# Optimization experiments

Measured on AMD Instinct MI355X. Metric: run time of the kernel, lower is better.

The kernel has to match this reference:

```python
import jax, jax.numpy as jnp
import numpy as np

N = 4096          # number of leaves
M = 2 * N - 1     # total tree nodes
B = 256           # batch of distribution pairs


def setup_inputs() -> dict:
    key = jax.random.key(0)
    k0, k1, k2, k3, k4, k5 = jax.random.split(key, 6)
    # ancestor-indicator matrix: mostly zeros (structured sparse used densely)
    subtree = (jax.random.uniform(k0, (M, N)) < 0.01).astype(jnp.float32)
    d1 = jax.random.uniform(k1, (N, B), dtype=jnp.float32)
    d2 = jax.random.uniform(k2, (N, B), dtype=jnp.float32)
    ot_distances = jax.random.uniform(k3, (B,), dtype=jnp.float32)
    param = jax.random.normal(k4, (M,), dtype=jnp.float32)
    parents = jax.random.randint(k5, (M,), 0, M, dtype=jnp.int32)
    return {"d1": d1, "d2": d2, "ot_distances": ot_distances,
            "subtree": subtree, "param": param, "parents": parents}


def reference(d1, d2, ot_distances, subtree, param, parents):
    # aggregate leaf mass to every tree node: [M, B]
    m_d1 = jnp.matmul(subtree, d1)
    m_d2 = jnp.matmul(subtree, d2)
    # edge weight = parent height - node height: [M]
    w_v = param[parents] - param
    # tree-Wasserstein-1 per pair: [B]
    w1_tree = 0.5 * jnp.matmul(w_v, jnp.abs(m_d1 - m_d2))
    return jnp.sum(jnp.square(ot_distances - w1_tree))
```

## Files before the change

### kernel.cpp

```cpp
#include <hip/hip_runtime.h>

#define NN    4096
#define MM    8191
#define BB    256
#define CAP   256

__device__ __forceinline__ int prefix_lt(unsigned long long m) {
    return __builtin_amdgcn_mbcnt_hi((unsigned)(m >> 32),
           __builtin_amdgcn_mbcnt_lo((unsigned)m, 0u));
}

__device__ __forceinline__ unsigned pack2bf(float lo, float hi) {
    unsigned a = __float_as_uint(lo);
    unsigned b = __float_as_uint(hi);
    a += 0x7fffu + ((a >> 16) & 1u);
    b += 0x7fffu + ((b >> 16) & 1u);
    return (a >> 16) | (b & 0xffff0000u);
}

__global__ __launch_bounds__(256) void k_prep(const float4* __restrict__ d1,
                                              const float4* __restrict__ d2,
                                              float* __restrict__ part2,
                                              uint2* __restrict__ ddp) {
    int idx = blockIdx.x * 256 + threadIdx.x;
    if (idx < 256 * BB) part2[idx] = 0.0f;
    float4 a = d1[idx], b = d2[idx];
    uint2 r;
    r.x = pack2bf(a.x - b.x, a.y - b.y);
    r.y = pack2bf(a.z - b.z, a.w - b.w);
    ddp[idx] = r;
}

__global__ __launch_bounds__(256, 4) void k_fused(
        const float4* __restrict__ st4,
        const uint2* __restrict__ ddp,
        const float* __restrict__ param,
        const int*   __restrict__ parents,
        float* __restrict__ part2) {
    __shared__ unsigned short s_idx[4][CAP];
    __shared__ float s_part[BB];
    const int tid  = threadIdx.x;
    const int wave = tid >> 6;
    const int lane = tid & 63;
    unsigned short* buf = s_idx[wave];

    s_part[tid] = 0.0f;
    __syncthreads();

    const int m = blockIdx.x * 4 + wave;
    if (m < MM) {
        int c = 0;
        #pragma unroll
        for (int h = 0; h < 2; ++h) {
            const float4* base = st4 + (size_t)m * (NN / 4) + h * (NN / 8);
            float4 v0 = base[lane];
            float4 v1 = base[64  + lane];
            float4 v2 = base[128 + lane];
            float4 v3 = base[192 + lane];
            float4 v4 = base[256 + lane];
            float4 v5 = base[320 + lane];
            float4 v6 = base[384 + lane];
            float4 v7 = base[448 + lane];

            const int cb = h * (NN / 2);
            #define SITE(val, col)                                          \
            {                                                               \
                unsigned long long mk = __ballot((val) != 0.0f);            \
                if ((val) != 0.0f)                                          \
                    buf[c + prefix_lt(mk)] = (unsigned short)(col);         \
                c += __popcll(mk);                                          \
            }
            #define QUAD(v, cb0)                                            \
                SITE(v.x, (cb0))     SITE(v.y, (cb0) + 1)                   \
                SITE(v.z, (cb0) + 2) SITE(v.w, (cb0) + 3)
            QUAD(v0, cb + (lane)       * 4)
            QUAD(v1, cb + (64  + lane) * 4)
            QUAD(v2, cb + (128 + lane) * 4)
            QUAD(v3, cb + (192 + lane) * 4)
            QUAD(v4, cb + (256 + lane) * 4)
            QUAD(v5, cb + (320 + lane) * 4)
            QUAD(v6, cb + (384 + lane) * 4)
            QUAD(v7, cb + (448 + lane) * 4)
            #undef QUAD
            #undef SITE
        }
        __builtin_amdgcn_wave_barrier();

        float c0 = 0.f, c1 = 0.f, c2 = 0.f, c3 = 0.f;
        float e0 = 0.f, e1 = 0.f, e2 = 0.f, e3 = 0.f;
        #define UNP0(u) __uint_as_float((u) << 16)
        #define UNP1(u) __uint_as_float((u) & 0xffff0000u)
        #define ACCA(g) { c0 += UNP0(g.x); c1 += UNP1(g.x); c2 += UNP0(g.y); c3 += UNP1(g.y); }
        #define ACCB(g) { e0 += UNP0(g.x); e1 += UNP1(g.x); e2 += UNP0(g.y); e3 += UNP1(g.y); }
        const unsigned* lw = (const unsigned*)buf;
        int i = 0;
        for (; i + 8 <= c; i += 8) {
            unsigned q0 = lw[(i >> 1)    ];
            unsigned q1 = lw[(i >> 1) + 1];
            unsigned q2 = lw[(i >> 1) + 2];
            unsigned q3 = lw[(i >> 1) + 3];
            unsigned o0 = (q0 & 0xffffu) * 64u + lane;
            unsigned o1 = (q0 >> 16)     * 64u + lane;
            unsigned o2 = (q1 & 0xffffu) * 64u + lane;
            unsigned o3 = (q1 >> 16)     * 64u + lane;
            unsigned o4 = (q2 & 0xffffu) * 64u + lane;
            unsigned o5 = (q2 >> 16)     * 64u + lane;
            unsigned o6 = (q3 & 0xffffu) * 64u + lane;
            unsigned o7 = (q3 >> 16)     * 64u + lane;
            uint2 g0 = ddp[o0];
            uint2 g1 = ddp[o1];
            uint2 g2 = ddp[o2];
            uint2 g3 = ddp[o3];
            uint2 g4 = ddp[o4];
            uint2 g5 = ddp[o5];
            uint2 g6 = ddp[o6];
            uint2 g7 = ddp[o7];
            ACCA(g0) ACCB(g1) ACCA(g2) ACCB(g3)
            ACCA(g4) ACCB(g5) ACCA(g6) ACCB(g7)
        }
        for (; i + 4 <= c; i += 4) {
            unsigned q0 = lw[(i >> 1)    ];
            unsigned q1 = lw[(i >> 1) + 1];
            unsigned o0 = (q0 & 0xffffu) * 64u + lane;
            unsigned o1 = (q0 >> 16)     * 64u + lane;
            unsigned o2 = (q1 & 0xffffu) * 64u + lane;
            unsigned o3 = (q1 >> 16)     * 64u + lane;
            uint2 g0 = ddp[o0];
            uint2 g1 = ddp[o1];
            uint2 g2 = ddp[o2];
            uint2 g3 = ddp[o3];
            ACCA(g0) ACCB(g1) ACCA(g2) ACCB(g3)
        }
        for (; i < c; ++i) {
            unsigned n = buf[i];
            uint2 g = ddp[n * 64u + lane];
            ACCA(g)
        }
        #undef ACCA
        #undef ACCB
        #undef UNP0
        #undef UNP1

        const float wgt = param[parents[m]] - param[m];
        atomicAdd(&s_part[4 * lane + 0], wgt * fabsf(c0 + e0));
        atomicAdd(&s_part[4 * lane + 1], wgt * fabsf(c1 + e1));
        atomicAdd(&s_part[4 * lane + 2], wgt * fabsf(c2 + e2));
        atomicAdd(&s_part[4 * lane + 3], wgt * fabsf(c3 + e3));
    }
    __syncthreads();
    atomicAdd(&part2[(size_t)(blockIdx.x & 255) * BB + tid], s_part[tid]);
}

__global__ __launch_bounds__(1024) void k_finalize(const float* __restrict__ part2,
                                                   const float* __restrict__ ot,
                                                   float* __restrict__ out) {
    __shared__ float s_red[4][BB];
    __shared__ float s_sq[16];
    const int tid = threadIdx.x;
    const int s = tid >> 8, b = tid & 255;

    float a0 = 0.f, a1 = 0.f, a2 = 0.f, a3 = 0.f;
    float a4 = 0.f, a5 = 0.f, a6 = 0.f, a7 = 0.f;
    #pragma unroll
    for (int j = 0; j < 64; j += 8) {
        int row = s * 64 + j;
        a0 += part2[(row    ) * BB + b];
        a1 += part2[(row + 1) * BB + b];
        a2 += part2[(row + 2) * BB + b];
        a3 += part2[(row + 3) * BB + b];
        a4 += part2[(row + 4) * BB + b];
        a5 += part2[(row + 5) * BB + b];
        a6 += part2[(row + 6) * BB + b];
        a7 += part2[(row + 7) * BB + b];
    }
    s_red[s][b] = ((a0 + a1) + (a2 + a3)) + ((a4 + a5) + (a6 + a7));
    __syncthreads();

    float v = 0.0f;
    if (s == 0) {
        float w1 = (s_red[0][b] + s_red[1][b]) + (s_red[2][b] + s_red[3][b]);
        float e = ot[b] - 0.5f * w1;
        v = e * e;
    }
    #pragma unroll
    for (int off = 32; off > 0; off >>= 1) v += __shfl_down(v, off, 64);
    if ((tid & 63) == 0) s_sq[tid >> 6] = v;
    __syncthreads();
    if (tid == 0) out[0] = (s_sq[0] + s_sq[1]) + (s_sq[2] + s_sq[3]);
}

extern "C" void kernel_launch(void* const* d_in, const int* in_sizes, int n_in,
                              void* d_out, int out_size, void* d_ws, size_t ws_size,
                              hipStream_t stream) {
    const float* d1      = (const float*)d_in[0];
    const float* d2      = (const float*)d_in[1];
    const float* ot      = (const float*)d_in[2];
    const float* subtree = (const float*)d_in[3];
    const float* param   = (const float*)d_in[4];
    const int*   parents = (const int*)d_in[5];

    char* wsb = (char*)d_ws;
    float* part2 = (float*)wsb;
    uint2* ddp   = (uint2*)(wsb + 256 * BB * 4);

    k_prep<<<1024, 256, 0, stream>>>((const float4*)d1, (const float4*)d2,
                                     part2, ddp);
    k_fused<<<2048, 256, 0, stream>>>((const float4*)subtree, ddp,
                                      param, parents, part2);
    k_finalize<<<1, 1024, 0, stream>>>(part2, ot, (float*)d_out);
}
```

Measured before the change: 48.68 us.

## Make fused kernel persistent with double-buffered nontemporal subtree row loads

Shrinks the grid so each wave processes four rows, prefetching the next half-row of the subtree matrix into a second register set while compacting and gathering the current half. Subtree loads use nontemporal hints to avoid evicting the packed difference data used by the gathers. Per-row LDS atomics are replaced by register accumulation with a single atomic flush per wave. Fewer resident waves may reduce latency hiding, and register pressure rises from holding two row buffers.

```diff
diff --git a/kernel.cpp b/kernel.cpp
--- a/kernel.cpp
+++ b/kernel.cpp
@@ -4,6 +4,8 @@
 #define MM    8191
 #define BB    256
 #define CAP   256
+
+typedef float nfloat4 __attribute__((ext_vector_type(4)));
 
 __device__ __forceinline__ int prefix_lt(unsigned long long m) {
     return __builtin_amdgcn_mbcnt_hi((unsigned)(m >> 32),
@@ -32,7 +34,7 @@
 }
 
 __global__ __launch_bounds__(256, 4) void k_fused(
-        const float4* __restrict__ st4,
+        const nfloat4* __restrict__ st4,
         const uint2* __restrict__ ddp,
         const float* __restrict__ param,
         const int*   __restrict__ parents,
@@ -47,106 +49,137 @@
     s_part[tid] = 0.0f;
     __syncthreads();
 
-    const int m = blockIdx.x * 4 + wave;
-    if (m < MM) {
-        int c = 0;
-        #pragma unroll
-        for (int h = 0; h < 2; ++h) {
-            const float4* base = st4 + (size_t)m * (NN / 4) + h * (NN / 8);
-            float4 v0 = base[lane];
-            float4 v1 = base[64  + lane];
-            float4 v2 = base[128 + lane];
-            float4 v3 = base[192 + lane];
-            float4 v4 = base[256 + lane];
-            float4 v5 = base[320 + lane];
-            float4 v6 = base[384 + lane];
-            float4 v7 = base[448 + lane];
-
-            const int cb = h * (NN / 2);
-            #define SITE(val, col)                                          \
-            {                                                               \
-                unsigned long long mk = __ballot((val) != 0.0f);            \
-                if ((val) != 0.0f)                                          \
-                    buf[c + prefix_lt(mk)] = (unsigned short)(col);         \
-                c += __popcll(mk);                                          \
-            }
-            #define QUAD(v, cb0)                                            \
-                SITE(v.x, (cb0))     SITE(v.y, (cb0) + 1)                   \
-                SITE(v.z, (cb0) + 2) SITE(v.w, (cb0) + 3)
-            QUAD(v0, cb + (lane)       * 4)
-            QUAD(v1, cb + (64  + lane) * 4)
-            QUAD(v2, cb + (128 + lane) * 4)
-            QUAD(v3, cb + (192 + lane) * 4)
-            QUAD(v4, cb + (256 + lane) * 4)
-            QUAD(v5, cb + (320 + lane) * 4)
-            QUAD(v6, cb + (384 + lane) * 4)
-            QUAD(v7, cb + (448 + lane) * 4)
-            #undef QUAD
-            #undef SITE
-        }
-        __builtin_amdgcn_wave_barrier();
-
+    const int g = blockIdx.x * 4 + wave;
+    float p0 = 0.f, p1 = 0.f, p2 = 0.f, p3 = 0.f;
+
+    nfloat4 a0, a1, a2, a3, a4, a5, a6, a7;
+    nfloat4 b0, b1, b2, b3, b4, b5, b6, b7;
+
+    #define ISSUE(P, m, h)                                                   \
+    {                                                                        \
+        const nfloat4* base = st4 + (size_t)(m) * (NN / 4) + (h) * (NN / 8); \
+        P##0 = __builtin_nontemporal_load(base + lane);                      \
+        P##1 = __builtin_nontemporal_load(base + 64  + lane);                \
+        P##2 = __builtin_nontemporal_load(base + 128 + lane);                \
+        P##3 = __builtin_nontemporal_load(base + 192 + lane);                \
+        P##4 = __builtin_nontemporal_load(base + 256 + lane);                \
+        P##5 = __builtin_nontemporal_load(base + 320 + lane);                \
+        P##6 = __builtin_nontemporal_load(base + 384 + lane);                \
+        P##7 = __builtin_nontemporal_load(base + 448 + lane);                \
+    }
+    #define SITE(val, col)                                                   \
+    {                                                                        \
+        unsigned long long mk = __ballot((val) != 0.0f);                     \
+        if ((val) != 0.0f)                                                   \
+            buf[c + prefix_lt(mk)] = (unsigned short)(col);                  \
+        c += __popcll(mk);                                                   \
+    }
+    #define QUAD(v, cb0)                                                     \
+        SITE(v.x, (cb0))     SITE(v.y, (cb0) + 1)                            \
+        SITE(v.z, (cb0) + 2) SITE(v.w, (cb0) + 3)
+    #define COMPACT(P, h)                                                    \
+    {                                                                        \
+        const int cb = (h) * (NN / 2);                                       \
+        QUAD(P##0, cb + (lane)       * 4)                                    \
+        QUAD(P##1, cb + (64  + lane) * 4)                                    \
+        QUAD(P##2, cb + (128 + lane) * 4)                                    \
+        QUAD(P##3, cb + (192 + lane) * 4)                                    \
+        QUAD(P##4, cb + (256 + lane) * 4)                                    \
+        QUAD(P##5, cb + (320 + lane) * 4)                                    \
+        QUAD(P##6, cb + (384 + lane) * 4)                                    \
+        QUAD(P##7, cb + (448 + lane) * 4)                                    \
+    }
+    #define UNP0(u) __uint_as_float((u) << 16)
+    #define UNP1(u) __uint_as_float((u) & 0xffff0000u)
+    #define ACCA(g) { c0 += UNP0(g.x); c1 += UNP1(g.x); c2 += UNP0(g.y); c3 += UNP1(g.y); }
+    #define ACCB(g) { e0 += UNP0(g.x); e1 += UNP1(g.x); e2 += UNP0(g.y); e3 += UNP1(g.y); }
+    #define GATHER                                                           \
+    {                                                                        \
+        const unsigned* lw = (const unsigned*)buf;                           \
+        int i = 0;                                                           \
+        for (; i + 8 <= c; i += 8) {                                         \
+            unsigned q0 = lw[(i >> 1)    ];                                  \
+            unsigned q1 = lw[(i >> 1) + 1];                                  \
+            unsigned q2 = lw[(i >> 1) + 2];                                  \
+            unsigned q3 = lw[(i >> 1) + 3];                                  \
+            unsigned o0 = (q0 & 0xffffu) * 64u + lane;                       \
+            unsigned o1 = (q0 >> 16)     * 64u + lane;                       \
+            unsigned o2 = (q1 & 0xffffu) * 64u + lane;                       \
+            unsigned o3 = (q1 >> 16)     * 64u + lane;                       \
+            unsigned o4 = (q2 & 0xffffu) * 64u + lane;                       \
+            unsigned o5 = (q2 >> 16)     * 64u + lane;                       \
+            unsigned o6 = (q3 & 0xffffu) * 64u + lane;                       \
+            unsigned o7 = (q3 >> 16)     * 64u + lane;                       \
+            uint2 g0 = ddp[o0]; uint2 g1 = ddp[o1];                          \
+            uint2 g2 = ddp[o2]; uint2 g3 = ddp[o3];                          \
+            uint2 g4 = ddp[o4]; uint2 g5 = ddp[o5];                          \
+            uint2 g6 = ddp[o6]; uint2 g7 = ddp[o7];                          \
+            ACCA(g0) ACCB(g1) ACCA(g2) ACCB(g3)                              \
+            ACCA(g4) ACCB(g5) ACCA(g6) ACCB(g7)                              \
+        }                                                                    \
+        for (; i + 4 <= c; i += 4) {                                         \
+            unsigned q0 = lw[(i >> 1)    ];                                  \
+            unsigned q1 = lw[(i >> 1) + 1];                                  \
+            unsigned o0 = (q0 & 0xffffu) * 64u + lane;                       \
+            unsigned o1 = (q0 >> 16)     * 64u + lane;                       \
+            unsigned o2 = (q1 & 0xffffu) * 64u + lane;                       \
+            unsigned o3 = (q1 >> 16)     * 64u + lane;                       \
+            uint2 g0 = ddp[o0]; uint2 g1 = ddp[o1];                          \
+            uint2 g2 = ddp[o2]; uint2 g3 = ddp[o3];                          \
+            ACCA(g0) ACCB(g1) ACCA(g2) ACCB(g3)                              \
+        }                                                                    \
+        for (; i < c; ++i) {                                                 \
+            unsigned n = buf[i];                                             \
+            uint2 g = ddp[n * 64u + lane];                                   \
+            ACCA(g)                                                          \
+        }                                                                    \
+    }
+    #define WB __builtin_amdgcn_wave_barrier()
+
+    ISSUE(a, g, 0);
+    #pragma unroll 1
+    for (int k = 0; k < 4; ++k) {
+        const int m = g + k * 2048;
+        if (m >= MM) break;
         float c0 = 0.f, c1 = 0.f, c2 = 0.f, c3 = 0.f;
         float e0 = 0.f, e1 = 0.f, e2 = 0.f, e3 = 0.f;
-        #define UNP0(u) __uint_as_float((u) << 16)
-        #define UNP1(u) __uint_as_float((u) & 0xffff0000u)
-        #define ACCA(g) { c0 += UNP0(g.x); c1 += UNP1(g.x); c2 += UNP0(g.y); c3 += UNP1(g.y); }
-        #define ACCB(g) { e0 += UNP0(g.x); e1 += UNP1(g.x); e2 += UNP0(g.y); e3 += UNP1(g.y); }
-        const unsigned* lw = (const unsigned*)buf;
-        int i = 0;
-        for (; i + 8 <= c; i += 8) {
-            unsigned q0 = lw[(i >> 1)    ];
-            unsigned q1 = lw[(i >> 1) + 1];
-            unsigned q2 = lw[(i >> 1) + 2];
-            unsigned q3 = lw[(i >> 1) + 3];
-            unsigned o0 = (q0 & 0xffffu) * 64u + lane;
-            unsigned o1 = (q0 >> 16)     * 64u + lane;
-            unsigned o2 = (q1 & 0xffffu) * 64u + lane;
-            unsigned o3 = (q1 >> 16)     * 64u + lane;
-            unsigned o4 = (q2 & 0xffffu) * 64u + lane;
-            unsigned o5 = (q2 >> 16)     * 64u + lane;
-            unsigned o6 = (q3 & 0xffffu) * 64u + lane;
-            unsigned o7 = (q3 >> 16)     * 64u + lane;
-            uint2 g0 = ddp[o0];
-            uint2 g1 = ddp[o1];
-            uint2 g2 = ddp[o2];
-            uint2 g3 = ddp[o3];
-            uint2 g4 = ddp[o4];
-            uint2 g5 = ddp[o5];
-            uint2 g6 = ddp[o6];
-            uint2 g7 = ddp[o7];
-            ACCA(g0) ACCB(g1) ACCA(g2) ACCB(g3)
-            ACCA(g4) ACCB(g5) ACCA(g6) ACCB(g7)
-        }
-        for (; i + 4 <= c; i += 4) {
-            unsigned q0 = lw[(i >> 1)    ];
-            unsigned q1 = lw[(i >> 1) + 1];
-            unsigned o0 = (q0 & 0xffffu) * 64u + lane;
-            unsigned o1 = (q0 >> 16)     * 64u + lane;
-            unsigned o2 = (q1 & 0xffffu) * 64u + lane;
-            unsigned o3 = (q1 >> 16)     * 64u + lane;
-            uint2 g0 = ddp[o0];
-            uint2 g1 = ddp[o1];
-            uint2 g2 = ddp[o2];
-            uint2 g3 = ddp[o3];
-            ACCA(g0) ACCB(g1) ACCA(g2) ACCB(g3)
-        }
-        for (; i < c; ++i) {
-            unsigned n = buf[i];
-            uint2 g = ddp[n * 64u + lane];
-            ACCA(g)
-        }
-        #undef ACCA
-        #undef ACCB
-        #undef UNP0
-        #undef UNP1
+
+        ISSUE(b, m, 1);
+        int c = 0;
+        COMPACT(a, 0);
+        WB;
+        GATHER;
+        WB;
+
+        const int mn = m + 2048;
+        if (mn < MM) ISSUE(a, mn, 0);
+        c = 0;
+        COMPACT(b, 1);
+        WB;
+        GATHER;
+        WB;
 
         const float wgt = param[parents[m]] - param[m];
-        atomicAdd(&s_part[4 * lane + 0], wgt * fabsf(c0 + e0));
-        atomicAdd(&s_part[4 * lane + 1], wgt * fabsf(c1 + e1));
-        atomicAdd(&s_part[4 * lane + 2], wgt * fabsf(c2 + e2));
-        atomicAdd(&s_part[4 * lane + 3], wgt * fabsf(c3 + e3));
-    }
+        p0 += wgt * fabsf(c0 + e0);
+        p1 += wgt * fabsf(c1 + e1);
+        p2 += wgt * fabsf(c2 + e2);
+        p3 += wgt * fabsf(c3 + e3);
+    }
+    #undef WB
+    #undef GATHER
+    #undef ACCA
+    #undef ACCB
+    #undef UNP0
+    #undef UNP1
+    #undef COMPACT
+    #undef QUAD
+    #undef SITE
+    #undef ISSUE
+
+    atomicAdd(&s_part[4 * lane + 0], p0);
+    atomicAdd(&s_part[4 * lane + 1], p1);
+    atomicAdd(&s_part[4 * lane + 2], p2);
+    atomicAdd(&s_part[4 * lane + 3], p3);
     __syncthreads();
     atomicAdd(&part2[(size_t)(blockIdx.x & 255) * BB + tid], s_part[tid]);
 }
@@ -205,7 +238,7 @@
 
     k_prep<<<1024, 256, 0, stream>>>((const float4*)d1, (const float4*)d2,
                                      part2, ddp);
-    k_fused<<<2048, 256, 0, stream>>>((const float4*)subtree, ddp,
-                                      param, parents, part2);
+    k_fused<<<512, 256, 0, stream>>>((const nfloat4*)subtree, ddp,
+                                     param, parents, part2);
     k_finalize<<<1, 1024, 0, stream>>>(part2, ot, (float*)d_out);
 }
```

Measured after the change: 53.82 us. +10.6%, slower.
